# Performance work log

Hardware: AMD Instinct MI355X
Metric: run time of the kernel (lower is better)

## Reference

```python
import jax, jax.numpy as jnp
import numpy as np

B, S, DDENSE, D, V, F, K = 8192, 26, 13, 32, 100000, 8, 7


def setup_inputs() -> dict:
    key = jax.random.key(0)
    ks = jax.random.split(key, 24)
    n = lambda i, shape, s=0.05: (jax.random.normal(ks[i], shape, dtype=jnp.float32) * s)
    return {
        'sparse_inputs': jax.random.randint(ks[0], (B, S), 0, V),
        'dense_inputs': jax.random.normal(ks[1], (B, DDENSE), dtype=jnp.float32),
        'gen_table': n(2, (V, D), 0.1), 'gen_W': n(3, (DDENSE, D)), 'gen_b': jnp.zeros((D,), jnp.float32),
        'cls_table': n(4, (V, D), 0.1), 'cls_W': n(5, (DDENSE, D)), 'cls_b': jnp.zeros((D,), jnp.float32),
        'conv_k0': n(6, (K, 1, 1, F)), 'conv_b0': jnp.zeros((F,), jnp.float32),
        'fc_W0': n(7, (13 * D * F, 3 * D)), 'fc_b0': jnp.zeros((3 * D,), jnp.float32),
        'conv_k1': n(8, (K, 1, F, F)), 'conv_b1': jnp.zeros((F,), jnp.float32),
        'fc_W1': n(9, (6 * D * F, 3 * D)), 'fc_b1': jnp.zeros((3 * D,), jnp.float32),
        'mlp_W1': n(10, (1584, 128)), 'mlp_b1': jnp.zeros((128,), jnp.float32),
        'bn_gamma': jnp.ones((128,), jnp.float32), 'bn_beta': jnp.zeros((128,), jnp.float32),
        'bn_mean': jnp.zeros((128,), jnp.float32), 'bn_var': jnp.ones((128,), jnp.float32),
        'out_W': n(11, (128, 1)), 'out_b': jnp.zeros((1,), jnp.float32),
    }


def _embed(sparse_inputs, dense_inputs, table, W, b):
    sp = table[sparse_inputs]                       # [B, 26, 32]
    dn = (dense_inputs @ W + b)[:, None, :]         # [B, 1, 32]
    return jnp.concatenate([sp, dn], axis=1)        # [B, 27, 32]


def _conv_tanh(x, k, b):
    y = jax.lax.conv_general_dilated(x, k, (1, 1), 'SAME',
                                     dimension_numbers=('NHWC', 'HWIO', 'NHWC'))
    return jnp.tanh(y + b)


def _maxpool2(x):  # MaxPooling2D((2,1), padding='valid') on NHWC
    return jax.lax.reduce_window(x, -jnp.inf, jax.lax.max,
                                 (1, 2, 1, 1), (1, 2, 1, 1), 'VALID')


def _forward(sparse_inputs, dense_inputs, gen_table, gen_W, gen_b,
             cls_table, cls_W, cls_b, conv_k0, conv_b0, fc_W0, fc_b0,
             conv_k1, conv_b1, fc_W1, fc_b1, mlp_W1, mlp_b1,
             bn_gamma, bn_beta, bn_mean, bn_var, out_W, out_b):
    embs_gen = _embed(sparse_inputs, dense_inputs, gen_table, gen_W, gen_b)
    embs_cls = _embed(sparse_inputs, dense_inputs, cls_table, cls_W, cls_b)

    x = embs_gen[..., None]                         # [B, 27, 32, 1] NHWC
    new_feats = []
    for ck, cb, fw, fb in ((conv_k0, conv_b0, fc_W0, fc_b0),
                           (conv_k1, conv_b1, fc_W1, fc_b1)):
        x = _maxpool2(_conv_tanh(x, ck, cb))
        flat = x.reshape(x.shape[0], -1)
        new_feats.append(jnp.tanh(flat @ fw + fb))  # [B, 96]

    gen = jnp.concatenate(new_feats, axis=1).reshape(x.shape[0], -1, D)  # [B, 6, 32]
    aug = jnp.concatenate([embs_cls, gen], axis=1)                       # [B, 33, 32]

    # pairwise inner products = upper triangle of Gram matrix, combinations order
    gram = jnp.einsum('bnd,bmd->bnm', aug, aug)
    iu, ju = jnp.triu_indices(aug.shape[1], k=1)
    ip = gram[:, iu, ju]                            # [B, 528]

    h = jnp.concatenate([ip, aug.reshape(aug.shape[0], -1)], axis=1)     # [B, 1584]
    h = jax.nn.relu(h @ mlp_W1 + mlp_b1)
    h = (h - bn_mean) * jax.lax.rsqrt(bn_var + 1e-3) * bn_gamma + bn_beta
    return jax.nn.sigmoid(h @ out_W + out_b)        # [B, 1]


def reference(sparse_inputs, dense_inputs, gen_table, gen_W, gen_b,
              cls_table, cls_W, cls_b, conv_k0, conv_b0, fc_W0, fc_b0,
              conv_k1, conv_b1, fc_W1, fc_b1, mlp_W1, mlp_b1,
              bn_gamma, bn_beta, bn_mean, bn_var, out_W, out_b):
    return _forward(sparse_inputs, dense_inputs, gen_table, gen_W, gen_b,
                    cls_table, cls_W, cls_b, conv_k0, conv_b0, fc_W0, fc_b0,
                    conv_k1, conv_b1, fc_W1, fc_b1, mlp_W1, mlp_b1,
                    bn_gamma, bn_beta, bn_mean, bn_var, out_W, out_b)
```

## Files before the change

kernel.cpp:

```cpp
#include <hip/hip_runtime.h>
#include <hip/hip_bf16.h>
#include <math.h>

#define BATCH 8192

typedef unsigned short bf16_t;
typedef _Float16 f16_t;
typedef __attribute__((ext_vector_type(2))) _Float16 h2_t;
typedef __attribute__((ext_vector_type(8))) short short8;
typedef __attribute__((ext_vector_type(4))) float f32x4;

union U32H2 { unsigned int u; h2_t h; };

__device__ __forceinline__ float bf2f(bf16_t u) {
    union { unsigned int i; float f; } v; v.i = ((unsigned int)u) << 16; return v.f;
}
__device__ __forceinline__ bf16_t f2bf(float f) {
    union { float f; unsigned int i; } v; v.f = f;
    unsigned int x = v.i;
    unsigned int r = (x + 0x7FFFu + ((x >> 16) & 1u)) >> 16;
    return (bf16_t)r;
}
__device__ __forceinline__ float fast_tanh(float x) {
    float ax = fabsf(x);
    float e = __expf(ax + ax);
    float t = 1.0f - 2.0f * __builtin_amdgcn_rcpf(e + 1.0f);
    return copysignf(t, x);
}

__global__ __launch_bounds__(256) void k_wtrans(
    const float* __restrict__ W0, const float* __restrict__ W1, const float* __restrict__ W2,
    bf16_t* __restrict__ Wt0, bf16_t* __restrict__ Wt1, bf16_t* __restrict__ Wt2)
{
    __shared__ float tile[64 * 129];
    const int m = blockIdx.y, t = threadIdx.x;
    const float* src; bf16_t* dst; int Ks, Kd, N, tiles;
    if (m == 0)      { src = W0; dst = Wt0; Ks = 3328; Kd = 3328; N = 96;  tiles = 52; }
    else if (m == 1) { src = W1; dst = Wt1; Ks = 1536; Kd = 1536; N = 96;  tiles = 24; }
    else             { src = W2; dst = Wt2; Ks = 1584; Kd = 1600; N = 128; tiles = 25; }
    if (blockIdx.x >= tiles) return;
    const int k0 = blockIdx.x * 64;
    const int nv = N >> 2;
    for (int i = t; i < 64 * nv; i += 256) {
        int r = i / nv, c4 = i - r * nv;
        int k = k0 + r;
        float4 v = make_float4(0.f, 0.f, 0.f, 0.f);
        if (k < Ks) v = *(const float4*)(src + (size_t)k * N + c4 * 4);
        tile[r * 129 + c4 * 4 + 0] = v.x;
        tile[r * 129 + c4 * 4 + 1] = v.y;
        tile[r * 129 + c4 * 4 + 2] = v.z;
        tile[r * 129 + c4 * 4 + 3] = v.w;
    }
    __syncthreads();
    for (int i = t; i < N * 32; i += 256) {
        int n = i >> 5, j = i & 31;
        unsigned int pk = (unsigned int)f2bf(tile[(2 * j) * 129 + n])
                        | ((unsigned int)f2bf(tile[(2 * j + 1) * 129 + n]) << 16);
        *(unsigned int*)(dst + (size_t)n * Kd + k0 + 2 * j) = pk;
    }
}

__global__ __launch_bounds__(256) void k_conv_fused(
    const int* __restrict__ sp, const float* __restrict__ dn,
    const float* __restrict__ gen_table, const float* __restrict__ gen_W, const float* __restrict__ gen_b,
    const float* __restrict__ k0, const float* __restrict__ b0,
    const float* __restrict__ k1, const float* __restrict__ b1,
    bf16_t* __restrict__ pooled0, bf16_t* __restrict__ pooled1)
{
    __shared__ float embGt[2][32][28];
    __shared__ unsigned int x0[2 * 13 * 32 * 4];
    __shared__ float k0s[56], k1s[448], b0s[8], b1s[8];
    __shared__ int ids[52];
    __shared__ float dloc[26];
    const int t = threadIdx.x;
    const int half = t >> 7, tt = t & 127;
    const int b = blockIdx.x * 2 + half;

    if (tt < 26) ids[half * 26 + tt] = sp[b * 26 + tt];
    if (tt >= 32 && tt < 45) dloc[half * 13 + tt - 32] = dn[b * 13 + (tt - 32)];
    if (t < 56) k0s[t] = k0[t];
    if (t >= 64 && t < 72) b0s[t - 64] = b0[t - 64];
    if (t >= 72 && t < 80) b1s[t - 72] = b1[t - 72];
    for (int i = t; i < 448; i += 256) k1s[i] = k1[i];
    __syncthreads();

    for (int i = tt; i < 416; i += 128) {
        int s_ = i >> 4, d = (i & 15) * 2;
        float2 v = *(const float2*)(gen_table + (size_t)ids[half * 26 + s_] * 32 + d);
        embGt[half][d][s_] = v.x;
        embGt[half][d + 1][s_] = v.y;
    }
    if (tt < 32) {
        float a = gen_b[tt];
        #pragma unroll
        for (int k = 0; k < 13; k++) a += dloc[half * 13 + k] * gen_W[k * 32 + tt];
        embGt[half][tt][26] = a;
    }
    __syncthreads();

    {
        const int w = tt >> 2, f0 = (tt & 3) * 2;
        const float* xp = &embGt[half][w][0];
        float xr[28];
        #pragma unroll
        for (int q = 0; q < 7; q++) {
            float4 v = *(const float4*)(xp + 4 * q);
            xr[4 * q] = v.x; xr[4 * q + 1] = v.y; xr[4 * q + 2] = v.z; xr[4 * q + 3] = v.w;
        }
        float k0r[7][2];
        #pragma unroll
        for (int tap = 0; tap < 7; tap++) {
            k0r[tap][0] = k0s[tap * 8 + f0];
            k0r[tap][1] = k0s[tap * 8 + f0 + 1];
        }
        const float b00 = b0s[f0], b01 = b0s[f0 + 1];
        #pragma unroll
        for (int hp = 0; hp < 13; hp++) {
            float p00 = b00, p01 = b01, p10 = b00, p11 = b01;
            #pragma unroll
            for (int tap = 0; tap < 7; tap++) {
                const int h0 = 2 * hp + tap - 3;
                if (h0 >= 0 && h0 < 27) {
                    p00 += xr[h0] * k0r[tap][0];
                    p01 += xr[h0] * k0r[tap][1];
                }
                const int h1 = 2 * hp + 1 + tap - 3;
                if (h1 >= 0 && h1 < 27) {
                    p10 += xr[h1] * k0r[tap][0];
                    p11 += xr[h1] * k0r[tap][1];
                }
            }
            float m0 = fast_tanh(fmaxf(p00, p10));
            float m1 = fast_tanh(fmaxf(p01, p11));
            unsigned int pk = (unsigned int)f2bf(m0) | ((unsigned int)f2bf(m1) << 16);
            *(unsigned int*)(pooled0 + (size_t)b * 3328 + hp * 256 + w * 8 + f0) = pk;
            U32H2 hx; hx.h = h2_t{(f16_t)m0, (f16_t)m1};
            x0[half * 1664 + hp * 128 + w * 4 + (tt & 3)] = hx.u;
        }
    }
    __syncthreads();

    {
        const int w1 = t >> 3, fo = t & 7;
        h2_t kh[7][4];
        #pragma unroll
        for (int tap = 0; tap < 7; tap++)
            #pragma unroll
            for (int q = 0; q < 4; q++)
                kh[tap][q] = h2_t{(f16_t)k1s[tap * 64 + (2 * q) * 8 + fo],
                                  (f16_t)k1s[tap * 64 + (2 * q + 1) * 8 + fo]};
        const f16_t bbh = (f16_t)b1s[fo];

        #pragma unroll
        for (int s = 0; s < 2; s++) {
            h2_t acc[12];
            #pragma unroll
            for (int r = 0; r < 12; r++) acc[r] = h2_t{bbh, (f16_t)0.f};
            #pragma unroll
            for (int hh = 0; hh < 13; hh++) {
                uint4 v = *(const uint4*)&x0[s * 1664 + hh * 128 + w1 * 4];
                U32H2 c0, c1, c2, c3;
                c0.u = v.x; c1.u = v.y; c2.u = v.z; c3.u = v.w;
                h2_t x2[4] = { c0.h, c1.h, c2.h, c3.h };
                #pragma unroll
                for (int tap = 0; tap < 7; tap++) {
                    const int r = hh + 3 - tap;
                    if (r >= 0 && r < 12) {
                        #pragma unroll
                        for (int q = 0; q < 4; q++) acc[r] += x2[q] * kh[tap][q];
                    }
                }
            }
            const int bs = blockIdx.x * 2 + s;
            #pragma unroll
            for (int hp = 0; hp < 6; hp++) {
                float a0 = (float)acc[2 * hp][0] + (float)acc[2 * hp][1];
                float a1 = (float)acc[2 * hp + 1][0] + (float)acc[2 * hp + 1][1];
                float m = fast_tanh(fmaxf(a0, a1));
                pooled1[(size_t)bs * 1536 + hp * 256 + w1 * 8 + fo] = f2bf(m);
            }
        }
    }
}

__global__ __launch_bounds__(256) void k_fc_mfma(
    const bf16_t* __restrict__ A0, const bf16_t* __restrict__ Wt0, float* __restrict__ P0,
    const bf16_t* __restrict__ A1, const bf16_t* __restrict__ Wt1, float* __restrict__ P1)
{
    const int which = blockIdx.z;
    const bf16_t* A  = which ? A1 : A0;
    const bf16_t* Wt = which ? Wt1 : Wt0;
    float* P = (which ? P1 : P0) + (size_t)blockIdx.y * (BATCH * 96);
    const int K = which ? 1536 : 3328;
    const int iters = which ? 12 : 26;

    const int t = threadIdx.x, w = t >> 6, l = t & 63;
    const int lane15 = l & 15, quad = l >> 4;
    const int rowA = blockIdx.x * 64 + w * 16 + lane15;
    const int kb = blockIdx.y * (K >> 2);

    const bf16_t* ap = A + (size_t)rowA * K + kb + quad * 8;
    const bf16_t* wp = Wt + (size_t)lane15 * K + kb + quad * 8;
    const size_t wstride = (size_t)16 * K;
    f32x4 acc[6] = {};

    #pragma unroll 2
    for (int it = 0; it < iters; it++) {
        short8 a = *(const short8*)(ap + it * 32);
        #pragma unroll
        for (int nt = 0; nt < 6; nt++) {
            short8 bf = *(const short8*)(wp + nt * wstride + it * 32);
            acc[nt] = __builtin_amdgcn_mfma_f32_16x16x32_bf16(a, bf, acc[nt], 0, 0, 0);
        }
    }
    const int baser = blockIdx.x * 64 + w * 16 + quad * 4;
    #pragma unroll
    for (int nt = 0; nt < 6; nt++)
        #pragma unroll
        for (int i = 0; i < 4; i++)
            P[(size_t)(baser + i) * 96 + nt * 16 + lane15] = acc[nt][i];
}

__global__ __launch_bounds__(256) void k_build_h(
    const int* __restrict__ sp, const float* __restrict__ dn,
    const float* __restrict__ cls_table, const float* __restrict__ cls_W, const float* __restrict__ cls_b,
    const float* __restrict__ p0, const float* __restrict__ fb0,
    const float* __restrict__ p1, const float* __restrict__ fb1,
    bf16_t* __restrict__ h)
{
    __shared__ bf16_t augs[4][33][40];
    __shared__ float grams[4][32][34];
    const int t = threadIdx.x, wv = t >> 6, l = t & 63;
    const int b = blockIdx.x * 4 + wv;
    bf16_t (*aug)[40] = augs[wv];
    float (*gram)[34] = grams[wv];

    const int myid = (l < 26) ? sp[b * 26 + l] : 0;

    for (int i = l; i < 416; i += 64) {
        int s_ = i >> 4, d = (i & 15) * 2;
        int id = __shfl(myid, s_);
        float2 v = *(const float2*)(cls_table + (size_t)id * 32 + d);
        unsigned int pk = (unsigned int)f2bf(v.x) | ((unsigned int)f2bf(v.y) << 16);
        *(unsigned int*)&aug[s_][d] = pk;
    }
    if (l < 32) {
        float a = cls_b[l];
        #pragma unroll
        for (int k = 0; k < 13; k++) a += dn[b * 13 + k] * cls_W[k * 32 + l];
        aug[26][l] = f2bf(a);
    }
    for (int i = l; i < 192; i += 64) {
        int n = 27 + (i >> 5), d = i & 31;
        float s;
        if (i < 96) {
            size_t o = (size_t)b * 96 + i;
            s = p0[o] + p0[o + 786432] + p0[o + 2 * 786432] + p0[o + 3 * 786432] + fb0[i];
        } else {
            int j = i - 96; size_t o = (size_t)b * 96 + j;
            s = p1[o] + p1[o + 786432] + p1[o + 2 * 786432] + p1[o + 3 * 786432] + fb1[j];
        }
        aug[n][d] = f2bf(fast_tanh(s));
    }

    const int m16 = l & 15, quad = l >> 4;
    short8 a0 = *(const short8*)&aug[m16][quad * 8];
    short8 a1 = *(const short8*)&aug[16 + m16][quad * 8];
    f32x4 c00 = {}, c01 = {}, c11 = {};
    c00 = __builtin_amdgcn_mfma_f32_16x16x32_bf16(a0, a0, c00, 0, 0, 0);
    c01 = __builtin_amdgcn_mfma_f32_16x16x32_bf16(a0, a1, c01, 0, 0, 0);
    c11 = __builtin_amdgcn_mfma_f32_16x16x32_bf16(a1, a1, c11, 0, 0, 0);
    #pragma unroll
    for (int i = 0; i < 4; i++) {
        gram[quad * 4 + i][m16] = c00[i];
        gram[quad * 4 + i][16 + m16] = c01[i];
        gram[16 + quad * 4 + i][16 + m16] = c11[i];
    }
    if (l < 32) {
        float s = 0.f;
        #pragma unroll
        for (int kk = 0; kk < 16; kk++) {
            unsigned int x = *(const unsigned int*)&aug[l][2 * kk];
            unsigned int y = *(const unsigned int*)&aug[32][2 * kk];
            s += bf2f((bf16_t)(x & 0xFFFFu)) * bf2f((bf16_t)(y & 0xFFFFu));
            s += bf2f((bf16_t)(x >> 16)) * bf2f((bf16_t)(y >> 16));
        }
        gram[l][32] = s;
    }

    bf16_t* hb = h + (size_t)b * 1600;
    for (int idx = l; idx < 528; idx += 64) {
        int n = idx >> 4, d = (idx & 15) * 2;
        *(unsigned int*)(hb + 528 + 2 * idx) = *(const unsigned int*)&aug[n][d];
    }
    if (l < 8) *(unsigned int*)(hb + 1584 + 2 * l) = 0u;
    for (int pp = l; pp < 264; pp += 64) {
        int p = 2 * pp;
        int i = (int)((65.0f - sqrtf(4225.0f - 8.0f * (float)p)) * 0.5f);
        int st = (i * (65 - i)) >> 1;
        if (st > p) { i--; st = (i * (65 - i)) >> 1; }
        else { int st2 = ((i + 1) * (64 - i)) >> 1; if (st2 <= p) { i++; st = st2; } }
        int j = i + 1 + (p - st);
        float s0, s1;
        if (j < 32) { s0 = gram[i][j]; s1 = gram[i][j + 1]; }
        else        { s0 = gram[i][32]; s1 = gram[i + 1][i + 2]; }
        unsigned int pk = (unsigned int)f2bf(s0) | ((unsigned int)f2bf(s1) << 16);
        *(unsigned int*)(hb + p) = pk;
    }
}

__global__ __launch_bounds__(256) void k_mlp_mfma(
    const bf16_t* __restrict__ h, const bf16_t* __restrict__ Wt2,
    const float* __restrict__ b1, const float* __restrict__ gamma,
    const float* __restrict__ beta, const float* __restrict__ mean,
    const float* __restrict__ var, const float* __restrict__ outW,
    const float* __restrict__ outb, float* __restrict__ out)
{
    __shared__ float lds[2 * 16 * 65];
    __shared__ float red2[32];
    const int t = threadIdx.x, w = t >> 6, l = t & 63;
    const int lane15 = l & 15, quad = l >> 4;
    const int nhalf = w & 1, khalf = w >> 1;
    const int rowA = blockIdx.x * 16 + lane15;

    const bf16_t* ap = h + (size_t)rowA * 1600 + khalf * 800 + quad * 8;
    f32x4 acc[4] = {};

    #pragma unroll 2
    for (int it = 0; it < 25; it++) {
        short8 a = *(const short8*)(ap + it * 32);
        #pragma unroll
        for (int nt = 0; nt < 4; nt++) {
            int n = nhalf * 64 + nt * 16 + lane15;
            short8 bf = *(const short8*)(Wt2 + (size_t)n * 1600 + khalf * 800 + it * 32 + quad * 8);
            acc[nt] = __builtin_amdgcn_mfma_f32_16x16x32_bf16(a, bf, acc[nt], 0, 0, 0);
        }
    }

    if (khalf == 1) {
        #pragma unroll
        for (int nt = 0; nt < 4; nt++)
            #pragma unroll
            for (int i = 0; i < 4; i++)
                lds[nhalf * 1040 + (quad * 4 + i) * 65 + nt * 16 + lane15] = acc[nt][i];
    }
    __syncthreads();
    if (khalf == 0) {
        float pl[4] = { 0.f, 0.f, 0.f, 0.f };
        #pragma unroll
        for (int nt = 0; nt < 4; nt++) {
            int c = nhalf * 64 + nt * 16 + lane15;
            float sc = gamma[c] * rsqrtf(var[c] + 1e-3f);
            float sh = beta[c] - mean[c] * sc;
            float ow = outW[c], bb = b1[c];
            #pragma unroll
            for (int i = 0; i < 4; i++) {
                float v = acc[nt][i] + lds[nhalf * 1040 + (quad * 4 + i) * 65 + nt * 16 + lane15] + bb;
                v = fmaxf(v, 0.f);
                pl[i] += (v * sc + sh) * ow;
            }
        }
        #pragma unroll
        for (int m = 1; m < 16; m <<= 1)
            #pragma unroll
            for (int i = 0; i < 4; i++) pl[i] += __shfl_xor(pl[i], m);
        if (lane15 == 0) {
            #pragma unroll
            for (int i = 0; i < 4; i++) red2[(quad * 4 + i) * 2 + nhalf] = pl[i];
        }
    }
    __syncthreads();
    if (t < 16) {
        float s = red2[t * 2] + red2[t * 2 + 1] + outb[0];
        out[blockIdx.x * 16 + t] = 1.f / (1.f + __expf(-s));
    }
}

extern "C" void kernel_launch(void* const* d_in, const int* in_sizes, int n_in,
                              void* d_out, int out_size, void* d_ws, size_t ws_size,
                              hipStream_t stream) {
    const int*   sp       = (const int*)d_in[0];
    const float* dn       = (const float*)d_in[1];
    const float* gen_tab  = (const float*)d_in[2];
    const float* gen_W    = (const float*)d_in[3];
    const float* gen_b    = (const float*)d_in[4];
    const float* cls_tab  = (const float*)d_in[5];
    const float* cls_W    = (const float*)d_in[6];
    const float* cls_b    = (const float*)d_in[7];
    const float* conv_k0  = (const float*)d_in[8];
    const float* conv_b0  = (const float*)d_in[9];
    const float* fc_W0    = (const float*)d_in[10];
    const float* fc_b0    = (const float*)d_in[11];
    const float* conv_k1  = (const float*)d_in[12];
    const float* conv_b1  = (const float*)d_in[13];
    const float* fc_W1    = (const float*)d_in[14];
    const float* fc_b1    = (const float*)d_in[15];
    const float* mlp_W1   = (const float*)d_in[16];
    const float* mlp_b1   = (const float*)d_in[17];
    const float* bn_gamma = (const float*)d_in[18];
    const float* bn_beta  = (const float*)d_in[19];
    const float* bn_mean  = (const float*)d_in[20];
    const float* bn_var   = (const float*)d_in[21];
    const float* out_W    = (const float*)d_in[22];
    const float* out_b    = (const float*)d_in[23];
    float* out = (float*)d_out;

    char* ws = (char*)d_ws;
    bf16_t* pooled0 = (bf16_t*)(ws + 0);
    bf16_t* pooled1 = (bf16_t*)(ws + 54525952ULL);
    float*  p0      = (float*)(ws + 79691776ULL);
    float*  p1      = (float*)(ws + 92274688ULL);
    bf16_t* Wt0     = (bf16_t*)(ws + 104857600ULL);
    bf16_t* Wt1     = (bf16_t*)(ws + 105496576ULL);
    bf16_t* Wt2     = (bf16_t*)(ws + 105791488ULL);
    bf16_t* h       = (bf16_t*)(ws + 0);

    k_wtrans<<<dim3(52, 3), 256, 0, stream>>>(fc_W0, fc_W1, mlp_W1, Wt0, Wt1, Wt2);
    k_conv_fused<<<BATCH / 2, 256, 0, stream>>>(sp, dn, gen_tab, gen_W, gen_b,
                                                conv_k0, conv_b0, conv_k1, conv_b1,
                                                pooled0, pooled1);
    k_fc_mfma<<<dim3(BATCH / 64, 4, 2), 256, 0, stream>>>(pooled0, Wt0, p0, pooled1, Wt1, p1);
    k_build_h<<<BATCH / 4, 256, 0, stream>>>(sp, dn, cls_tab, cls_W, cls_b,
                                             p0, fc_b0, p1, fc_b1, h);
    k_mlp_mfma<<<BATCH / 16, 256, 0, stream>>>(h, Wt2, mlp_b1, bn_gamma, bn_beta,
                                               bn_mean, bn_var, out_W, out_b, out);
}
```

Measured before the change: 287.6 us.

## Store activations and weights in MFMA-fragment tiled layout for contiguous wave loads

Activations (pooled0, pooled1, h) are now written in a 16-row by 8-k tiled layout, and weights are pre-packed into per-lane MFMA fragment order. Each wavefront's short8 loads in the FC and MLP GEMMs then read a contiguous 1 KB chunk instead of 16 rows strided by K. The aim is better coalescing and fewer cache lines per load. The cost is scattered, poorly coalesced scalar stores in the new weight-pack kernel and less contiguous 4-byte stores from the conv and build_h producers.

```diff
diff --git a/kernel.cpp b/kernel.cpp
--- a/kernel.cpp
+++ b/kernel.cpp
@@ -28,36 +28,27 @@
     return copysignf(t, x);
 }
 
-__global__ __launch_bounds__(256) void k_wtrans(
+
+__device__ __forceinline__ void wpack_one(
+    const float* __restrict__ src, bf16_t* __restrict__ dst,
+    int P, int N, int NT, int Ksrc)
+{
+    int e = P & 7, lane = (P >> 3) & 63, idx = P >> 9;
+    int nt = idx % NT, git = idx / NT;
+    int n = nt * 16 + (lane & 15);
+    int k = git * 32 + (lane >> 4) * 8 + e;
+    dst[P] = (k < Ksrc) ? f2bf(src[(size_t)k * N + n]) : (bf16_t)0;
+}
+
+__global__ __launch_bounds__(256) void k_wpack(
     const float* __restrict__ W0, const float* __restrict__ W1, const float* __restrict__ W2,
     bf16_t* __restrict__ Wt0, bf16_t* __restrict__ Wt1, bf16_t* __restrict__ Wt2)
 {
-    __shared__ float tile[64 * 129];
-    const int m = blockIdx.y, t = threadIdx.x;
-    const float* src; bf16_t* dst; int Ks, Kd, N, tiles;
-    if (m == 0)      { src = W0; dst = Wt0; Ks = 3328; Kd = 3328; N = 96;  tiles = 52; }
-    else if (m == 1) { src = W1; dst = Wt1; Ks = 1536; Kd = 1536; N = 96;  tiles = 24; }
-    else             { src = W2; dst = Wt2; Ks = 1584; Kd = 1600; N = 128; tiles = 25; }
-    if (blockIdx.x >= tiles) return;
-    const int k0 = blockIdx.x * 64;
-    const int nv = N >> 2;
-    for (int i = t; i < 64 * nv; i += 256) {
-        int r = i / nv, c4 = i - r * nv;
-        int k = k0 + r;
-        float4 v = make_float4(0.f, 0.f, 0.f, 0.f);
-        if (k < Ks) v = *(const float4*)(src + (size_t)k * N + c4 * 4);
-        tile[r * 129 + c4 * 4 + 0] = v.x;
-        tile[r * 129 + c4 * 4 + 1] = v.y;
-        tile[r * 129 + c4 * 4 + 2] = v.z;
-        tile[r * 129 + c4 * 4 + 3] = v.w;
-    }
-    __syncthreads();
-    for (int i = t; i < N * 32; i += 256) {
-        int n = i >> 5, j = i & 31;
-        unsigned int pk = (unsigned int)f2bf(tile[(2 * j) * 129 + n])
-                        | ((unsigned int)f2bf(tile[(2 * j + 1) * 129 + n]) << 16);
-        *(unsigned int*)(dst + (size_t)n * Kd + k0 + 2 * j) = pk;
-    }
+    const int m = blockIdx.y;
+    const int P = blockIdx.x * 256 + threadIdx.x;
+    if (m == 0)      { if (P < 319488) wpack_one(W0, Wt0, P, 96, 6, 3328); }
+    else if (m == 1) { if (P < 147456) wpack_one(W1, Wt1, P, 96, 6, 1536); }
+    else             { if (P < 204800) wpack_one(W2, Wt2, P, 128, 8, 1584); }
 }
 
 __global__ __launch_bounds__(256) void k_conv_fused(
@@ -97,6 +88,8 @@
         embGt[half][tt][26] = a;
     }
     __syncthreads();
+
+    bf16_t* p0base = pooled0 + ((size_t)(b >> 4) * 416) * 128 + (b & 15) * 8;
 
     {
         const int w = tt >> 2, f0 = (tt & 3) * 2;
@@ -133,7 +126,7 @@
             float m0 = fast_tanh(fmaxf(p00, p10));
             float m1 = fast_tanh(fmaxf(p01, p11));
             unsigned int pk = (unsigned int)f2bf(m0) | ((unsigned int)f2bf(m1) << 16);
-            *(unsigned int*)(pooled0 + (size_t)b * 3328 + hp * 256 + w * 8 + f0) = pk;
+            *(unsigned int*)(p0base + (hp * 32 + w) * 128 + f0) = pk;
             U32H2 hx; hx.h = h2_t{(f16_t)m0, (f16_t)m1};
             x0[half * 1664 + hp * 128 + w * 4 + (tt & 3)] = hx.u;
         }
@@ -172,12 +165,13 @@
                 }
             }
             const int bs = blockIdx.x * 2 + s;
+            bf16_t* p1base = pooled1 + ((size_t)(bs >> 4) * 192) * 128 + (bs & 15) * 8;
             #pragma unroll
             for (int hp = 0; hp < 6; hp++) {
                 float a0 = (float)acc[2 * hp][0] + (float)acc[2 * hp][1];
                 float a1 = (float)acc[2 * hp + 1][0] + (float)acc[2 * hp + 1][1];
                 float m = fast_tanh(fmaxf(a0, a1));
-                pooled1[(size_t)bs * 1536 + hp * 256 + w1 * 8 + fo] = f2bf(m);
+                p1base[(hp * 32 + w1) * 128 + fo] = f2bf(m);
             }
         }
     }
@@ -196,20 +190,19 @@
 
     const int t = threadIdx.x, w = t >> 6, l = t & 63;
     const int lane15 = l & 15, quad = l >> 4;
-    const int rowA = blockIdx.x * 64 + w * 16 + lane15;
+    const int rb = blockIdx.x * 4 + w;
     const int kb = blockIdx.y * (K >> 2);
 
-    const bf16_t* ap = A + (size_t)rowA * K + kb + quad * 8;
-    const bf16_t* wp = Wt + (size_t)lane15 * K + kb + quad * 8;
-    const size_t wstride = (size_t)16 * K;
+    const bf16_t* ap = A + ((size_t)rb * (K >> 3) + (kb >> 3) + quad) * 128 + lane15 * 8;
+    const bf16_t* bp = Wt + (size_t)(kb >> 5) * 3072 + l * 8;
     f32x4 acc[6] = {};
 
     #pragma unroll 2
     for (int it = 0; it < iters; it++) {
-        short8 a = *(const short8*)(ap + it * 32);
+        short8 a = *(const short8*)(ap + it * 512);
         #pragma unroll
         for (int nt = 0; nt < 6; nt++) {
-            short8 bf = *(const short8*)(wp + nt * wstride + it * 32);
+            short8 bf = *(const short8*)(bp + it * 3072 + nt * 512);
             acc[nt] = __builtin_amdgcn_mfma_f32_16x16x32_bf16(a, bf, acc[nt], 0, 0, 0);
         }
     }
@@ -288,12 +281,15 @@
         gram[l][32] = s;
     }
 
-    bf16_t* hb = h + (size_t)b * 1600;
+    bf16_t* hbp = h + ((size_t)(b >> 4) * 200) * 128 + (b & 15) * 8;
     for (int idx = l; idx < 528; idx += 64) {
-        int n = idx >> 4, d = (idx & 15) * 2;
-        *(unsigned int*)(hb + 528 + 2 * idx) = *(const unsigned int*)&aug[n][d];
-    }
-    if (l < 8) *(unsigned int*)(hb + 1584 + 2 * l) = 0u;
+        int k = 528 + 2 * idx;
+        *(unsigned int*)(hbp + (k >> 3) * 128 + (k & 7)) = *(const unsigned int*)&aug[idx >> 4][(idx & 15) * 2];
+    }
+    if (l < 8) {
+        int k = 1584 + 2 * l;
+        *(unsigned int*)(hbp + (k >> 3) * 128 + (k & 7)) = 0u;
+    }
     for (int pp = l; pp < 264; pp += 64) {
         int p = 2 * pp;
         int i = (int)((65.0f - sqrtf(4225.0f - 8.0f * (float)p)) * 0.5f);
@@ -305,7 +301,7 @@
         if (j < 32) { s0 = gram[i][j]; s1 = gram[i][j + 1]; }
         else        { s0 = gram[i][32]; s1 = gram[i + 1][i + 2]; }
         unsigned int pk = (unsigned int)f2bf(s0) | ((unsigned int)f2bf(s1) << 16);
-        *(unsigned int*)(hb + p) = pk;
+        *(unsigned int*)(hbp + (p >> 3) * 128 + (p & 7)) = pk;
     }
 }
 
@@ -321,18 +317,17 @@
     const int t = threadIdx.x, w = t >> 6, l = t & 63;
     const int lane15 = l & 15, quad = l >> 4;
     const int nhalf = w & 1, khalf = w >> 1;
-    const int rowA = blockIdx.x * 16 + lane15;
-
-    const bf16_t* ap = h + (size_t)rowA * 1600 + khalf * 800 + quad * 8;
+
+    const bf16_t* ap = h + ((size_t)blockIdx.x * 200 + khalf * 100 + quad) * 128 + lane15 * 8;
+    const bf16_t* bp = Wt2 + ((size_t)khalf * 25 * 8 + nhalf * 4) * 512 + l * 8;
     f32x4 acc[4] = {};
 
     #pragma unroll 2
     for (int it = 0; it < 25; it++) {
-        short8 a = *(const short8*)(ap + it * 32);
+        short8 a = *(const short8*)(ap + it * 512);
         #pragma unroll
         for (int nt = 0; nt < 4; nt++) {
-            int n = nhalf * 64 + nt * 16 + lane15;
-            short8 bf = *(const short8*)(Wt2 + (size_t)n * 1600 + khalf * 800 + it * 32 + quad * 8);
+            short8 bf = *(const short8*)(bp + it * 4096 + nt * 512);
             acc[nt] = __builtin_amdgcn_mfma_f32_16x16x32_bf16(a, bf, acc[nt], 0, 0, 0);
         }
     }
@@ -415,7 +410,7 @@
     bf16_t* Wt2     = (bf16_t*)(ws + 105791488ULL);
     bf16_t* h       = (bf16_t*)(ws + 0);
 
-    k_wtrans<<<dim3(52, 3), 256, 0, stream>>>(fc_W0, fc_W1, mlp_W1, Wt0, Wt1, Wt2);
+    k_wpack<<<dim3(1248, 3), 256, 0, stream>>>(fc_W0, fc_W1, mlp_W1, Wt0, Wt1, Wt2);
     k_conv_fused<<<BATCH / 2, 256, 0, stream>>>(sp, dn, gen_tab, gen_W, gen_b,
                                                 conv_k0, conv_b0, conv_k1, conv_b1,
                                                 pooled0, pooled1);
```

Measured after the change: 248.5 us. 13.6% less time.
